# Performance work log

Hardware: AMD Instinct MI355X
Metric: run time of the kernel (lower is better)

Reference implementation:

```python
import jax, jax.numpy as jnp
import numpy as np

P = 4096          # n_patch (64x64 grid)
S = 64            # grid side
L = 9             # 9-neighbor window
E = 34            # attention embed dim (32 hidden + 2 coords)
H = 32            # hidden size
N_OBS = 10
N_PRED = 50


def _neighbor_flat_idx():
    idx = np.arange(P)
    r, c = idx // S, idx % S
    off = np.array([[-1,-1],[-1,0],[-1,1],[0,-1],[0,0],[0,1],[1,-1],[1,0],[1,1]])
    nr = (r[:, None] + off[:, 0]).reshape(S, S, L)
    nc = (c[:, None] + off[:, 1]).reshape(S, S, L)
    # boundary shift (as in the torch module)
    nr[0] += 1; nr[-1] -= 1
    nc[:, 0] += 1; nc[:, -1] -= 1
    return jnp.asarray((nr * S + nc).reshape(P, L))  # [P, 9] into patch dim


def _patch_label(B):
    coords = jnp.arange(S, dtype=jnp.float32) / S
    pl = jnp.stack(jnp.meshgrid(coords, coords, indexing='ij'), -1).reshape(P, 2)
    return jnp.broadcast_to(pl[:, None, :], (P, B, 2))  # [P, B, 2]


def setup_inputs() -> dict:
    key = jax.random.key(0)
    ks = jax.random.split(key, 8)
    s = 0.1
    return {
        'x': jax.random.normal(ks[0], (N_OBS, 2 * P, H), jnp.float32),
        'W_x2h': jax.random.normal(ks[1], (H, H), jnp.float32) * s,
        'b_x2h': jnp.zeros((H,), jnp.float32),
        'W_h2h': jax.random.normal(ks[2], (H, H), jnp.float32) * s,
        'b_h2h': jnp.zeros((H,), jnp.float32),
        'W_fc2': jax.random.normal(ks[3], (H, H), jnp.float32) * s,
        'b_fc2': jnp.zeros((H,), jnp.float32),
        'ln_g': jnp.ones((H,), jnp.float32),
        'ln_b': jnp.zeros((H,), jnp.float32),
        'W_fcsa': jax.random.normal(ks[4], (H, E), jnp.float32) * s,
        'b_fcsa': jnp.zeros((H,), jnp.float32),
        'W_in': jax.random.normal(ks[5], (3 * E, E), jnp.float32) * s,
        'b_in': jnp.zeros((3 * E,), jnp.float32),
        'W_out': jax.random.normal(ks[6], (E, E), jnp.float32) * s,
        'b_out': jnp.zeros((E,), jnp.float32),
    }


def reference(x, W_x2h, b_x2h, W_h2h, b_h2h, W_fc2, b_fc2, ln_g, ln_b,
              W_fcsa, b_fcsa, W_in, b_in, W_out, b_out):
    B = x.shape[1] // P
    N = B * P
    nbr = _neighbor_flat_idx()
    pl = _patch_label(B)

    def layernorm(y):
        mu = jnp.mean(y, -1, keepdims=True)
        var = jnp.mean((y - mu) ** 2, -1, keepdims=True)
        return (y - mu) * jax.lax.rsqrt(var + 1e-5) * ln_g + ln_b

    def mha(xa):  # [L, N, E] self-attention, 1 head
        qkv = xa @ W_in.T + b_in
        q, k, v = jnp.split(qkv, 3, axis=-1)
        scores = jnp.einsum('lne,mne->nlm', q, k) / jnp.sqrt(jnp.float32(E))
        w = jax.nn.softmax(scores, axis=-1)
        o = jnp.einsum('nlm,mne->lne', w, v)
        return o @ W_out.T + b_out

    def step(h, inp):
        h = jnp.tanh(inp @ W_x2h.T + b_x2h + h @ W_h2h.T + b_h2h)  # [N, H]
        hb = jnp.transpose(h.reshape(B, P, H), (1, 0, 2))          # [P, B, H]
        qin = jnp.concatenate([hb, pl], -1)                        # [P, B, E]
        nq = qin[nbr]                                              # [P, 9, B, E]
        xa = jnp.transpose(nq, (1, 2, 0, 3)).reshape(L, N, E)      # [9, N, E]
        ao = mha(xa)[4]                                            # center, [N, E]
        h = h + ao @ W_fcsa.T + b_fcsa
        pred = layernorm(h @ W_fc2.T + b_fc2)
        return h, pred

    h0 = jnp.zeros((N, H), x.dtype)
    h, preds_obs = jax.lax.scan(step, h0, x)                       # [10, N, H]

    def step_pred(carry, _):
        h, p = carry
        h, pnew = step(h, p)
        return (h, pnew), pnew

    _, preds_fut = jax.lax.scan(step_pred, (h, preds_obs[-1]), None,
                                length=N_PRED - 1)                 # [49, N, H]
    return jnp.concatenate([preds_obs, preds_fut], 0)              # [59, N, H]
```

## Files before the change

### kernel.cpp

```cpp
#include <hip/hip_runtime.h>

#define NROWS 8192
#define RPB   32
#define TPB   1024
#define NBLK  256

#define OFF_W1   0
#define OFF_W2   1024
#define OFF_WIN  2048
#define OFF_WFC2 5516
#define OFF_M    6540
#define OFF_B12  7628
#define OFF_BIN  7660
#define OFF_B2   7762
#define OFF_BFC2 7794
#define OFF_LNG  7826
#define OFF_LNB  7858
#define OFF_QKV0 8192
#define QKVN     (NROWS*102)
#define OFF_QKV1 (OFF_QKV0 + QKVN)
#define OFF_HNEW (OFF_QKV1 + QKVN)

__global__ __launch_bounds__(256) void setup_kernel(
    const float* __restrict__ W_x2h, const float* __restrict__ b_x2h,
    const float* __restrict__ W_h2h, const float* __restrict__ b_h2h,
    const float* __restrict__ W_fc2, const float* __restrict__ b_fc2,
    const float* __restrict__ ln_g,  const float* __restrict__ ln_b,
    const float* __restrict__ W_fcsa,const float* __restrict__ b_fcsa,
    const float* __restrict__ W_in,  const float* __restrict__ b_in,
    const float* __restrict__ W_out, const float* __restrict__ b_out,
    float* __restrict__ ws)
{
  int t = blockIdx.x*blockDim.x + threadIdx.x;
  int stride = gridDim.x*blockDim.x;
  for (int i=t;i<1024;i+=stride) ws[OFF_W1+i]   = W_x2h[i];
  for (int i=t;i<1024;i+=stride) ws[OFF_W2+i]   = W_h2h[i];
  for (int i=t;i<3468;i+=stride) ws[OFF_WIN+i]  = W_in[i];
  for (int i=t;i<1024;i+=stride) ws[OFF_WFC2+i] = W_fc2[i];
  for (int i=t;i<32;i+=stride)   ws[OFF_B12+i]  = b_x2h[i] + b_h2h[i];
  for (int i=t;i<102;i+=stride)  ws[OFF_BIN+i]  = b_in[i];
  for (int i=t;i<32;i+=stride)   ws[OFF_BFC2+i] = b_fc2[i];
  for (int i=t;i<32;i+=stride)   ws[OFF_LNG+i]  = ln_g[i];
  for (int i=t;i<32;i+=stride)   ws[OFF_LNB+i]  = ln_b[i];
  for (int idx=t; idx<1088; idx+=stride) {
    int j = idx/34, f = idx - j*34;
    float acc = 0.f;
    for (int e=0;e<34;++e)
      acc += W_fcsa[j*34+e] * W_out[e*34+f];
    ws[OFF_M+idx] = acc;
  }
  for (int j=t;j<32;j+=stride){
    float acc = b_fcsa[j];
    for (int e=0;e<34;++e) acc += W_fcsa[j*34+e] * b_out[e];
    ws[OFF_B2+j] = acc;
  }
}

__global__ __launch_bounds__(TPB) void step_kernel(
    const float* __restrict__ ws,
    const float* __restrict__ qkvR,
    float* __restrict__ qkvW,
    float* __restrict__ hnewG,
    const float* __restrict__ x,
    float* __restrict__ out,
    int stepB, int stepA)
{
  __shared__ float sW1[32][32], sW2[32][32], sWfc2[32][32];
  __shared__ float sM[32][36];
  __shared__ float sWin[102][36];
  __shared__ float sB12[32], sBin[102], sB2[32], sBfc2[32], sLng[32], sLnb[32];
  __shared__ float sS[RPB][13];
  __shared__ float sO[RPB][35];
  __shared__ float sHp[RPB][33];
  __shared__ float sG[RPB][33];
  __shared__ float sPred[RPB][33];
  __shared__ float sHn[RPB][33];
  __shared__ float sX[RPB][33];

  const int tid  = threadIdx.x;
  const int lr2  = tid & 31;
  const int slot = tid >> 5;
  const int base = blockIdx.x * RPB;
  const int r2   = base + lr2;
  const int b    = base >> 12;
  const int p    = base & 4095;
  const int gr   = p >> 6;
  const int gc0  = p & 63;
  const int c    = gc0 + lr2;
  const int br   = (gr < 1) ? 1 : ((gr > 62) ? 62 : gr);
  const int bc   = (c  < 1) ? 1 : ((c  > 62) ? 62 : c);

  {
    sW1  [tid>>5][tid&31] = ws[OFF_W1  +tid];
    sW2  [tid>>5][tid&31] = ws[OFF_W2  +tid];
    sWfc2[tid>>5][tid&31] = ws[OFF_WFC2+tid];
    for (int idx=tid; idx<1088; idx+=TPB){ int j=idx/34, e=idx-j*34; sM[j][e]=ws[OFF_M+idx]; }
    for (int idx=tid; idx<3468; idx+=TPB){ int e=idx/34, f=idx-e*34; sWin[e][f]=ws[OFF_WIN+idx]; }
    if (tid < 102)                    sBin [tid]     = ws[OFF_BIN +tid];
    else if (tid>=128 && tid<160)     sB12 [tid-128] = ws[OFF_B12 +tid-128];
    else if (tid>=160 && tid<192)     sB2  [tid-160] = ws[OFF_B2  +tid-160];
    else if (tid>=192 && tid<224)     sBfc2[tid-192] = ws[OFF_BFC2+tid-192];
    else if (tid>=224 && tid<256)     sLng [tid-224] = ws[OFF_LNG +tid-224];
    else if (tid>=256 && tid<288)     sLnb [tid-256] = ws[OFF_LNB +tid-256];
  }
  if (stepA >= 0 && stepA < 10) {
    size_t xbase = ((size_t)stepA*NROWS + base)*32;
    sX[tid>>5][tid&31] = x[xbase + tid];
  }
  if (stepB >= 0) {
    if (slot >= 16) {
      const int j0 = (slot-16)*2;
      sHp[lr2][j0]   = hnewG[(size_t)j0    *NROWS + r2];
      sHp[lr2][j0+1] = hnewG[(size_t)(j0+1)*NROWS + r2];
    } else if (slot < 9) {
      const int m  = slot;
      const int dr = m/3 - 1, dc = m - (m/3)*3 - 1;
      const int qrow = (b<<12) + (br<<6) + bc;
      const int nr_  = (b<<12) + ((br+dr)<<6) + (bc+dc);
      float acc = 0.f;
      #pragma unroll
      for (int e=0;e<34;++e)
        acc += qkvR[(size_t)e*NROWS + qrow] * qkvR[(size_t)(34+e)*NROWS + nr_];
      sS[lr2][m] = acc * 0.1714985851425088f;
    }
  } else {
    sHp[lr2][slot] = 0.f;
  }
  __syncthreads();

  if (stepB >= 0) {
    {
      float sc[9]; float mx = -1e30f;
      #pragma unroll
      for (int m=0;m<9;++m){ sc[m]=sS[lr2][m]; mx=fmaxf(mx,sc[m]); }
      float sum=0.f;
      #pragma unroll
      for (int m=0;m<9;++m){ sc[m]=__expf(sc[m]-mx); sum+=sc[m]; }
      float inv = 1.f/sum;
      float o0=0.f, o1=0.f;
      const bool e2ok = (slot < 2);
      #pragma unroll
      for (int m=0;m<9;++m){
        int dr = m/3 - 1, dc = m - (m/3)*3 - 1;
        int nr_ = (b<<12) + ((br+dr)<<6) + (bc+dc);
        float wm = sc[m]*inv;
        o0 += wm * qkvR[(size_t)(68+slot)*NROWS + nr_];
        if (e2ok) o1 += wm * qkvR[(size_t)(100+slot)*NROWS + nr_];
      }
      sO[lr2][slot] = o0;
      if (e2ok) sO[lr2][32+slot] = o1;
    }
    __syncthreads();
    {
      float a = sB2[slot];
      #pragma unroll
      for (int e=0;e<34;++e) a += sO[lr2][e] * sM[slot][e];
      sHp[lr2][slot] += a;
    }
    __syncthreads();
    {
      float g = sBfc2[slot];
      #pragma unroll
      for (int i=0;i<32;++i) g += sHp[lr2][i] * sWfc2[slot][i];
      sG[lr2][slot] = g;
    }
    __syncthreads();
    {
      float mu=0.f;
      #pragma unroll
      for (int i=0;i<32;++i) mu += sG[lr2][i];
      mu *= 0.03125f;
      float var=0.f;
      #pragma unroll
      for (int i=0;i<32;++i){ float d=sG[lr2][i]-mu; var += d*d; }
      var *= 0.03125f;
      float rs = rsqrtf(var + 1e-5f);
      sPred[lr2][slot] = (sG[lr2][slot]-mu)*rs*sLng[slot] + sLnb[slot];
    }
    __syncthreads();
    {
      size_t obase = ((size_t)stepB*NROWS + base)*32;
      out[obase + tid] = sPred[tid>>5][tid&31];
    }
  } else {
    __syncthreads(); __syncthreads(); __syncthreads(); __syncthreads();
  }

  if (stepA >= 0) {
    float a = sB12[slot];
    if (stepA < 10) {
      #pragma unroll
      for (int i=0;i<32;++i)
        a += sX[lr2][i]*sW1[slot][i] + sHp[lr2][i]*sW2[slot][i];
    } else {
      #pragma unroll
      for (int i=0;i<32;++i)
        a += sPred[lr2][i]*sW1[slot][i] + sHp[lr2][i]*sW2[slot][i];
    }
    {
      float t0 = tanhf(a);
      sHn[lr2][slot] = t0;
      hnewG[(size_t)slot*NROWS + r2] = t0;
    }
    __syncthreads();
    float hn[32];
    #pragma unroll
    for (int f=0;f<32;++f) hn[f]=sHn[lr2][f];
    const float pl0 = gr*0.015625f, pl1 = c*0.015625f;
    #pragma unroll
    for (int k=0;k<4;++k){
      int e = slot + 32*k;
      if (e < 102) {
        float acc = sBin[e];
        #pragma unroll
        for (int f=0;f<32;++f) acc += hn[f]*sWin[e][f];
        acc += pl0*sWin[e][32] + pl1*sWin[e][33];
        qkvW[(size_t)e*NROWS + r2] = acc;
      }
    }
  }
}

extern "C" void kernel_launch(void* const* d_in, const int* in_sizes, int n_in,
                              void* d_out, int out_size, void* d_ws, size_t ws_size,
                              hipStream_t stream) {
  const float* x     = (const float*)d_in[0];
  const float* W_x2h = (const float*)d_in[1];
  const float* b_x2h = (const float*)d_in[2];
  const float* W_h2h = (const float*)d_in[3];
  const float* b_h2h = (const float*)d_in[4];
  const float* W_fc2 = (const float*)d_in[5];
  const float* b_fc2 = (const float*)d_in[6];
  const float* ln_g  = (const float*)d_in[7];
  const float* ln_b  = (const float*)d_in[8];
  const float* W_fcsa= (const float*)d_in[9];
  const float* b_fcsa= (const float*)d_in[10];
  const float* W_in  = (const float*)d_in[11];
  const float* b_in  = (const float*)d_in[12];
  const float* W_out = (const float*)d_in[13];
  const float* b_out = (const float*)d_in[14];
  float* ws = (float*)d_ws;
  float* out = (float*)d_out;

  setup_kernel<<<8, 256, 0, stream>>>(W_x2h,b_x2h,W_h2h,b_h2h,W_fc2,b_fc2,ln_g,ln_b,
                                      W_fcsa,b_fcsa,W_in,b_in,W_out,b_out, ws);
  for (int i=0;i<60;++i){
    int stepB = i-1;
    int stepA = (i<=58)? i : -1;
    const float* qR = ws + OFF_QKV0 + (size_t)((i+1)&1)*QKVN;
    float*       qW = ws + OFF_QKV0 + (size_t)(i&1)*QKVN;
    step_kernel<<<NBLK, TPB, 0, stream>>>(ws, qR, qW, ws+OFF_HNEW, x, out, stepB, stepA);
  }
}
```

Before: 962.6 us.

## Fuse two recurrent steps per launch using halo recomputation in shared memory

Each launch now covers two time steps. Every block recomputes the first step over a 3x33 halo of cells around its own 32-cell row segment, keeping the halo's qkv in shared memory so the second step's neighbour attention needs no global exchange. This halves the number of kernel launches and the global round trips of qkv and hidden state, at the cost of redundant halo computation (about three times the cells in the first step) and much larger shared memory use, which may reduce occupancy. Hidden state is double-buffered in a row-major layout, and shared arrays are padded to reduce bank conflicts.

Measured after the change: 1.472 ms. 1.53x slower.

```diff
diff --git a/kernel.cpp b/kernel.cpp
--- a/kernel.cpp
+++ b/kernel.cpp
@@ -1,9 +1,11 @@
 #include <hip/hip_runtime.h>
 
 #define NROWS 8192
-#define RPB   32
 #define TPB   1024
 #define NBLK  256
+#define NCELL 99
+#define SCALE 0.1714985851425088f
+#define INV64 0.015625f
 
 #define OFF_W1   0
 #define OFF_W2   1024
@@ -18,8 +20,8 @@
 #define OFF_LNB  7858
 #define OFF_QKV0 8192
 #define QKVN     (NROWS*102)
-#define OFF_QKV1 (OFF_QKV0 + QKVN)
-#define OFF_HNEW (OFF_QKV1 + QKVN)
+#define HNN      (NROWS*32)
+#define OFF_HN0  (OFF_QKV0 + 2*QKVN)
 
 __global__ __launch_bounds__(256) void setup_kernel(
     const float* __restrict__ W_x2h, const float* __restrict__ b_x2h,
@@ -56,167 +58,295 @@
   }
 }
 
-__global__ __launch_bounds__(TPB) void step_kernel(
+__global__ __launch_bounds__(TPB) void fused2_kernel(
     const float* __restrict__ ws,
     const float* __restrict__ qkvR,
     float* __restrict__ qkvW,
-    float* __restrict__ hnewG,
+    const float* __restrict__ hnR,
+    float* __restrict__ hnW,
     const float* __restrict__ x,
     float* __restrict__ out,
-    int stepB, int stepA)
+    int l)
 {
-  __shared__ float sW1[32][32], sW2[32][32], sWfc2[32][32];
-  __shared__ float sM[32][36];
-  __shared__ float sWin[102][36];
+  __shared__ float sW1[32][33], sW2[32][33], sWfc2[32][33];
+  __shared__ float sM[32][35];
+  __shared__ float sWin[102][35];
   __shared__ float sB12[32], sBin[102], sB2[32], sBfc2[32], sLng[32], sLnb[32];
-  __shared__ float sS[RPB][13];
-  __shared__ float sO[RPB][35];
-  __shared__ float sHp[RPB][33];
-  __shared__ float sG[RPB][33];
-  __shared__ float sPred[RPB][33];
-  __shared__ float sHn[RPB][33];
-  __shared__ float sX[RPB][33];
-
-  const int tid  = threadIdx.x;
-  const int lr2  = tid & 31;
-  const int slot = tid >> 5;
-  const int base = blockIdx.x * RPB;
-  const int r2   = base + lr2;
-  const int b    = base >> 12;
-  const int p    = base & 4095;
-  const int gr   = p >> 6;
-  const int gc0  = p & 63;
-  const int c    = gc0 + lr2;
-  const int br   = (gr < 1) ? 1 : ((gr > 62) ? 62 : gr);
-  const int bc   = (c  < 1) ? 1 : ((c  > 62) ? 62 : c);
+  __shared__ float sHp  [32][NCELL];
+  __shared__ float sPredT[32][NCELL];
+  __shared__ float sHnT [32][NCELL];
+  __shared__ float sGT  [32][NCELL];
+  __shared__ float sS[NCELL][13];
+  __shared__ float uOX[36][102];
+  __shared__ float sX2[32][33];
+  __shared__ float sQKV2[3][102][37];
+
+  const int tid = threadIdx.x;
+  const int bid = blockIdx.x;
+  const int b   = bid >> 7;
+  const int gr  = (bid >> 1) & 63;
+  const int ch  = bid & 1;
+  const int c0  = ch << 5;
+  const int br  = (gr < 1) ? 1 : ((gr > 62) ? 62 : gr);
+  const int R0  = br - 1;
+  const int C0  = ch ? 31 : 0;
+  const int rr_own = gr - R0;
+  const int cc0 = c0 - C0;
+  const int ownbase = (b<<12) + (gr<<6) + c0;
+  const int sPrev = 2*l - 1, sEven = 2*l, sOdd = 2*l + 1;
+  const bool hasP1 = (l >= 1);
+  const bool hasP4 = (sOdd <= 58);
 
   {
-    sW1  [tid>>5][tid&31] = ws[OFF_W1  +tid];
-    sW2  [tid>>5][tid&31] = ws[OFF_W2  +tid];
-    sWfc2[tid>>5][tid&31] = ws[OFF_WFC2+tid];
-    for (int idx=tid; idx<1088; idx+=TPB){ int j=idx/34, e=idx-j*34; sM[j][e]=ws[OFF_M+idx]; }
-    for (int idx=tid; idx<3468; idx+=TPB){ int e=idx/34, f=idx-e*34; sWin[e][f]=ws[OFF_WIN+idx]; }
-    if (tid < 102)                    sBin [tid]     = ws[OFF_BIN +tid];
-    else if (tid>=128 && tid<160)     sB12 [tid-128] = ws[OFF_B12 +tid-128];
-    else if (tid>=160 && tid<192)     sB2  [tid-160] = ws[OFF_B2  +tid-160];
-    else if (tid>=192 && tid<224)     sBfc2[tid-192] = ws[OFF_BFC2+tid-192];
-    else if (tid>=224 && tid<256)     sLng [tid-224] = ws[OFF_LNG +tid-224];
-    else if (tid>=256 && tid<288)     sLnb [tid-256] = ws[OFF_LNB +tid-256];
-  }
-  if (stepA >= 0 && stepA < 10) {
-    size_t xbase = ((size_t)stepA*NROWS + base)*32;
-    sX[tid>>5][tid&31] = x[xbase + tid];
-  }
-  if (stepB >= 0) {
-    if (slot >= 16) {
-      const int j0 = (slot-16)*2;
-      sHp[lr2][j0]   = hnewG[(size_t)j0    *NROWS + r2];
-      sHp[lr2][j0+1] = hnewG[(size_t)(j0+1)*NROWS + r2];
-    } else if (slot < 9) {
-      const int m  = slot;
-      const int dr = m/3 - 1, dc = m - (m/3)*3 - 1;
-      const int qrow = (b<<12) + (br<<6) + bc;
-      const int nr_  = (b<<12) + ((br+dr)<<6) + (bc+dc);
+    int j = tid >> 5, i = tid & 31;
+    sW1[j][i]   = ws[OFF_W1  + tid];
+    sW2[j][i]   = ws[OFF_W2  + tid];
+    sWfc2[j][i] = ws[OFF_WFC2+ tid];
+    for (int idx = tid; idx < 1088; idx += TPB){ int jj=idx/34, e=idx-jj*34; sM[jj][e]=ws[OFF_M+idx]; }
+    for (int idx = tid; idx < 3468; idx += TPB){ int e=idx/34, f=idx-e*34; sWin[e][f]=ws[OFF_WIN+idx]; }
+    if (tid < 102)                sBin [tid]     = ws[OFF_BIN + tid];
+    else if (tid>=128 && tid<160) sB12 [tid-128] = ws[OFF_B12 + tid-128];
+    else if (tid>=160 && tid<192) sB2  [tid-160] = ws[OFF_B2  + tid-160];
+    else if (tid>=192 && tid<224) sBfc2[tid-192] = ws[OFF_BFC2+ tid-192];
+    else if (tid>=224 && tid<256) sLng [tid-224] = ws[OFF_LNG + tid-224];
+    else if (tid>=256 && tid<288) sLnb [tid-256] = ws[OFF_LNB + tid-256];
+  }
+  if (l == 0) {
+    for (int tt = tid; tt < 3168; tt += TPB) {
+      int cell = tt >> 5, j = tt & 31;
+      sHp[j][cell] = 0.f;
+      int rr = cell/33, cc = cell - rr*33;
+      int ar = (b<<12) + ((R0+rr)<<6) + C0 + cc;
+      uOX[j][cell] = x[(size_t)ar*32 + j];
+    }
+  }
+  if (hasP4 && sOdd < 10) {
+    int cell = tid >> 5, j = tid & 31;
+    sX2[cell][j] = x[((size_t)sOdd*NROWS + ownbase + cell)*32 + j];
+  }
+  __syncthreads();
+
+  if (hasP1) {
+    if (tid < 891) {
+      int m = tid / 99, cell = tid - m*99;
+      int rr = cell/33, cc = cell - rr*33;
+      int g = R0+rr, c = C0+cc;
+      int bg  = (g<1)?1:((g>62)?62:g);
+      int bcc = (c<1)?1:((c>62)?62:c);
+      int dr = m/3 - 1, dc = m - (m/3)*3 - 1;
+      int qrow = (b<<12)+(bg<<6)+bcc;
+      int krow = (b<<12)+((bg+dr)<<6)+(bcc+dc);
       float acc = 0.f;
       #pragma unroll
       for (int e=0;e<34;++e)
-        acc += qkvR[(size_t)e*NROWS + qrow] * qkvR[(size_t)(34+e)*NROWS + nr_];
-      sS[lr2][m] = acc * 0.1714985851425088f;
-    }
-  } else {
-    sHp[lr2][slot] = 0.f;
-  }
-  __syncthreads();
-
-  if (stepB >= 0) {
-    {
+        acc += qkvR[(size_t)e*NROWS+qrow]*qkvR[(size_t)(34+e)*NROWS+krow];
+      sS[cell][m] = acc*SCALE;
+    }
+    __syncthreads();
+    if (tid < 990) {
+      int sub = tid / 99, cell = tid - sub*99;
+      int rr = cell/33, cc = cell - rr*33;
+      int g = R0+rr, c = C0+cc;
+      int bg  = (g<1)?1:((g>62)?62:g);
+      int bcc = (c<1)?1:((c>62)?62:c);
       float sc[9]; float mx = -1e30f;
       #pragma unroll
-      for (int m=0;m<9;++m){ sc[m]=sS[lr2][m]; mx=fmaxf(mx,sc[m]); }
+      for (int m=0;m<9;++m){ sc[m]=sS[cell][m]; mx=fmaxf(mx,sc[m]); }
       float sum=0.f;
       #pragma unroll
       for (int m=0;m<9;++m){ sc[m]=__expf(sc[m]-mx); sum+=sc[m]; }
       float inv = 1.f/sum;
-      float o0=0.f, o1=0.f;
-      const bool e2ok = (slot < 2);
+      const int f0=sub, f1=sub+10, f2=sub+20, f3=sub+30;
+      const bool h3 = (sub < 4);
+      float o0=0.f,o1=0.f,o2=0.f,o3=0.f;
       #pragma unroll
       for (int m=0;m<9;++m){
         int dr = m/3 - 1, dc = m - (m/3)*3 - 1;
-        int nr_ = (b<<12) + ((br+dr)<<6) + (bc+dc);
+        int krow = (b<<12)+((bg+dr)<<6)+(bcc+dc);
         float wm = sc[m]*inv;
-        o0 += wm * qkvR[(size_t)(68+slot)*NROWS + nr_];
-        if (e2ok) o1 += wm * qkvR[(size_t)(100+slot)*NROWS + nr_];
-      }
-      sO[lr2][slot] = o0;
-      if (e2ok) sO[lr2][32+slot] = o1;
-    }
-    __syncthreads();
-    {
-      float a = sB2[slot];
-      #pragma unroll
-      for (int e=0;e<34;++e) a += sO[lr2][e] * sM[slot][e];
-      sHp[lr2][slot] += a;
-    }
-    __syncthreads();
-    {
-      float g = sBfc2[slot];
-      #pragma unroll
-      for (int i=0;i<32;++i) g += sHp[lr2][i] * sWfc2[slot][i];
-      sG[lr2][slot] = g;
-    }
-    __syncthreads();
-    {
+        o0 += wm*qkvR[(size_t)(68+f0)*NROWS+krow];
+        o1 += wm*qkvR[(size_t)(68+f1)*NROWS+krow];
+        o2 += wm*qkvR[(size_t)(68+f2)*NROWS+krow];
+        if (h3) o3 += wm*qkvR[(size_t)(68+f3)*NROWS+krow];
+      }
+      uOX[f0][cell]=o0; uOX[f1][cell]=o1; uOX[f2][cell]=o2;
+      if (h3) uOX[f3][cell]=o3;
+    }
+    __syncthreads();
+    for (int tt = tid; tt < 3168; tt += TPB) {
+      int cell = tt>>5, j = tt&31;
+      int rr = cell/33, cc = cell - rr*33;
+      int ar = (b<<12)+((R0+rr)<<6)+C0+cc;
+      float a = sB2[j] + hnR[(size_t)ar*32 + j];
+      #pragma unroll
+      for (int e=0;e<34;++e) a += uOX[e][cell]*sM[j][e];
+      sHp[j][cell] = a;
+    }
+    __syncthreads();
+    for (int tt = tid; tt < 3168; tt += TPB) {
+      int cell = tt>>5, j = tt&31;
+      float g2 = sBfc2[j];
+      #pragma unroll
+      for (int i=0;i<32;++i) g2 += sHp[i][cell]*sWfc2[j][i];
+      sGT[j][cell] = g2;
+      if (sEven < 10) {
+        int rr = cell/33, cc = cell - rr*33;
+        int ar = (b<<12)+((R0+rr)<<6)+C0+cc;
+        uOX[j][cell] = x[((size_t)sEven*NROWS + ar)*32 + j];
+      }
+    }
+    __syncthreads();
+    for (int tt = tid; tt < 3168; tt += TPB) {
+      int cell = tt>>5, j = tt&31;
       float mu=0.f;
       #pragma unroll
-      for (int i=0;i<32;++i) mu += sG[lr2][i];
+      for (int i=0;i<32;++i) mu += sGT[i][cell];
       mu *= 0.03125f;
       float var=0.f;
       #pragma unroll
-      for (int i=0;i<32;++i){ float d=sG[lr2][i]-mu; var += d*d; }
+      for (int i=0;i<32;++i){ float d=sGT[i][cell]-mu; var += d*d; }
       var *= 0.03125f;
       float rs = rsqrtf(var + 1e-5f);
-      sPred[lr2][slot] = (sG[lr2][slot]-mu)*rs*sLng[slot] + sLnb[slot];
+      sPredT[j][cell] = (sGT[j][cell]-mu)*rs*sLng[j] + sLnb[j];
+    }
+    __syncthreads();
+  }
+
+  {
+    if (hasP1) {
+      int cell = tid>>5, j = tid&31;
+      int cellh = rr_own*33 + cc0 + cell;
+      out[((size_t)sPrev*NROWS + ownbase + cell)*32 + j] = sPredT[j][cellh];
+    }
+    for (int tt = tid; tt < 3168; tt += TPB) {
+      int cell = tt>>5, j = tt&31;
+      float a = sB12[j];
+      if (sEven < 10) {
+        #pragma unroll
+        for (int i=0;i<32;++i) a += uOX[i][cell]*sW1[j][i] + sHp[i][cell]*sW2[j][i];
+      } else {
+        #pragma unroll
+        for (int i=0;i<32;++i) a += sPredT[i][cell]*sW1[j][i] + sHp[i][cell]*sW2[j][i];
+      }
+      sHnT[j][cell] = tanhf(a);
+    }
+    __syncthreads();
+    for (int tt = tid; tt < 10098; tt += TPB) {
+      int e = tt / 99, cell = tt - e*99;
+      int rr = cell/33, cc = cell - rr*33;
+      float acc = sBin[e];
+      #pragma unroll
+      for (int f=0; f<32; ++f) acc += sHnT[f][cell]*sWin[e][f];
+      acc += (R0+rr)*INV64*sWin[e][32] + (C0+cc)*INV64*sWin[e][33];
+      sQKV2[rr][e][cc] = acc;
+    }
+    __syncthreads();
+  }
+
+  {
+    if (tid < 288) {
+      int m = tid>>5, cell = tid&31;
+      int c = c0 + cell;
+      int bcc = (c<1)?1:((c>62)?62:c);
+      int dr = m/3 - 1, dc = m - (m/3)*3 - 1;
+      int colq = bcc - C0, colk = bcc + dc - C0, rrk = 1 + dr;
+      float acc = 0.f;
+      #pragma unroll
+      for (int e=0;e<34;++e) acc += sQKV2[1][e][colq]*sQKV2[rrk][34+e][colk];
+      sS[cell][m] = acc*SCALE;
+    }
+    __syncthreads();
+    if (tid < 320) {
+      int sub = tid>>5, cell = tid&31;
+      int c = c0 + cell;
+      int bcc = (c<1)?1:((c>62)?62:c);
+      float sc[9]; float mx = -1e30f;
+      #pragma unroll
+      for (int m=0;m<9;++m){ sc[m]=sS[cell][m]; mx=fmaxf(mx,sc[m]); }
+      float sum=0.f;
+      #pragma unroll
+      for (int m=0;m<9;++m){ sc[m]=__expf(sc[m]-mx); sum+=sc[m]; }
+      float inv = 1.f/sum;
+      const int f0=sub, f1=sub+10, f2=sub+20, f3=sub+30;
+      const bool h3 = (sub < 4);
+      float o0=0.f,o1=0.f,o2=0.f,o3=0.f;
+      #pragma unroll
+      for (int m=0;m<9;++m){
+        int dr = m/3 - 1, dc = m - (m/3)*3 - 1;
+        int colk = bcc + dc - C0, rrk = 1 + dr;
+        float wm = sc[m]*inv;
+        o0 += wm*sQKV2[rrk][68+f0][colk];
+        o1 += wm*sQKV2[rrk][68+f1][colk];
+        o2 += wm*sQKV2[rrk][68+f2][colk];
+        if (h3) o3 += wm*sQKV2[rrk][68+f3][colk];
+      }
+      uOX[f0][cell]=o0; uOX[f1][cell]=o1; uOX[f2][cell]=o2;
+      if (h3) uOX[f3][cell]=o3;
     }
     __syncthreads();
     {
-      size_t obase = ((size_t)stepB*NROWS + base)*32;
-      out[obase + tid] = sPred[tid>>5][tid&31];
-    }
-  } else {
-    __syncthreads(); __syncthreads(); __syncthreads(); __syncthreads();
-  }
-
-  if (stepA >= 0) {
-    float a = sB12[slot];
-    if (stepA < 10) {
-      #pragma unroll
-      for (int i=0;i<32;++i)
-        a += sX[lr2][i]*sW1[slot][i] + sHp[lr2][i]*sW2[slot][i];
-    } else {
-      #pragma unroll
-      for (int i=0;i<32;++i)
-        a += sPred[lr2][i]*sW1[slot][i] + sHp[lr2][i]*sW2[slot][i];
-    }
+      int cell = tid>>5, j = tid&31;
+      int cellh = rr_own*33 + cc0 + cell;
+      float a = sB2[j] + sHnT[j][cellh];
+      #pragma unroll
+      for (int e=0;e<34;++e) a += uOX[e][cell]*sM[j][e];
+      sHp[j][cellh] = a;
+    }
+    __syncthreads();
     {
-      float t0 = tanhf(a);
-      sHn[lr2][slot] = t0;
-      hnewG[(size_t)slot*NROWS + r2] = t0;
-    }
-    __syncthreads();
-    float hn[32];
-    #pragma unroll
-    for (int f=0;f<32;++f) hn[f]=sHn[lr2][f];
-    const float pl0 = gr*0.015625f, pl1 = c*0.015625f;
-    #pragma unroll
-    for (int k=0;k<4;++k){
-      int e = slot + 32*k;
-      if (e < 102) {
-        float acc = sBin[e];
+      int cell = tid>>5, j = tid&31;
+      int cellh = rr_own*33 + cc0 + cell;
+      float g2 = sBfc2[j];
+      #pragma unroll
+      for (int i=0;i<32;++i) g2 += sHp[i][cellh]*sWfc2[j][i];
+      sGT[j][cellh] = g2;
+    }
+    __syncthreads();
+    {
+      int cell = tid>>5, j = tid&31;
+      int cellh = rr_own*33 + cc0 + cell;
+      float mu=0.f;
+      #pragma unroll
+      for (int i=0;i<32;++i) mu += sGT[i][cellh];
+      mu *= 0.03125f;
+      float var=0.f;
+      #pragma unroll
+      for (int i=0;i<32;++i){ float d=sGT[i][cellh]-mu; var += d*d; }
+      var *= 0.03125f;
+      float rs = rsqrtf(var + 1e-5f);
+      sPredT[j][cellh] = (sGT[j][cellh]-mu)*rs*sLng[j] + sLnb[j];
+    }
+    __syncthreads();
+  }
+
+  {
+    int cell = tid>>5, j = tid&31;
+    int cellh = rr_own*33 + cc0 + cell;
+    out[((size_t)sEven*NROWS + ownbase + cell)*32 + j] = sPredT[j][cellh];
+    if (hasP4) {
+      float a = sB12[j];
+      if (sOdd < 10) {
         #pragma unroll
-        for (int f=0;f<32;++f) acc += hn[f]*sWin[e][f];
-        acc += pl0*sWin[e][32] + pl1*sWin[e][33];
-        qkvW[(size_t)e*NROWS + r2] = acc;
-      }
+        for (int i=0;i<32;++i) a += sX2[cell][i]*sW1[j][i] + sHp[i][cellh]*sW2[j][i];
+      } else {
+        #pragma unroll
+        for (int i=0;i<32;++i) a += sPredT[i][cellh]*sW1[j][i] + sHp[i][cellh]*sW2[j][i];
+      }
+      float tv = tanhf(a);
+      sHnT[j][cellh] = tv;
+      hnW[((size_t)ownbase + cell)*32 + j] = tv;
+    }
+  }
+  if (hasP4) {
+    __syncthreads();
+    for (int tt = tid; tt < 3264; tt += TPB) {
+      int e = tt>>5, cell = tt&31;
+      int cellh = rr_own*33 + cc0 + cell;
+      float acc = sBin[e];
+      #pragma unroll
+      for (int f=0;f<32;++f) acc += sHnT[f][cellh]*sWin[e][f];
+      acc += gr*INV64*sWin[e][32] + (c0+cell)*INV64*sWin[e][33];
+      qkvW[(size_t)e*NROWS + ownbase + cell] = acc;
     }
   }
 }
@@ -244,11 +374,11 @@
 
   setup_kernel<<<8, 256, 0, stream>>>(W_x2h,b_x2h,W_h2h,b_h2h,W_fc2,b_fc2,ln_g,ln_b,
                                       W_fcsa,b_fcsa,W_in,b_in,W_out,b_out, ws);
-  for (int i=0;i<60;++i){
-    int stepB = i-1;
-    int stepA = (i<=58)? i : -1;
-    const float* qR = ws + OFF_QKV0 + (size_t)((i+1)&1)*QKVN;
-    float*       qW = ws + OFF_QKV0 + (size_t)(i&1)*QKVN;
-    step_kernel<<<NBLK, TPB, 0, stream>>>(ws, qR, qW, ws+OFF_HNEW, x, out, stepB, stepA);
+  for (int l = 0; l < 30; ++l) {
+    const float* qR = ws + OFF_QKV0 + (size_t)((l+1)&1)*QKVN;
+    float*       qW = ws + OFF_QKV0 + (size_t)(l&1)*QKVN;
+    const float* hR = ws + OFF_HN0  + (size_t)((l+1)&1)*HNN;
+    float*       hW = ws + OFF_HN0  + (size_t)(l&1)*HNN;
+    fused2_kernel<<<NBLK, TPB, 0, stream>>>(ws, qR, qW, hR, hW, x, out, l);
   }
 }
```

## Remap threads so each wavefront owns two rows, replacing block barriers with wave-local fences

Applied to the files above, without the earlier changes.

Changes the thread mapping so that each 64-lane wavefront handles two full rows, with lane j as the feature index. Most __syncthreads are replaced by an LDS wait plus a scheduling barrier, and LayerNorm reductions are done with cross-lane shuffles. The hidden state layout becomes row-major for coalesced access, and shared weight arrays are padded to avoid bank conflicts. The trade-offs are that global qkv reads now use strided access per lane, and correctness rests on data being shared only within a wavefront.

Result: slower. 1.416 ms (+47.1%).

```diff
diff --git a/kernel.cpp b/kernel.cpp
--- a/kernel.cpp
+++ b/kernel.cpp
@@ -4,6 +4,11 @@
 #define RPB   32
 #define TPB   1024
 #define NBLK  256
+#define SCALE 0.1714985851425088f
+#define INV64 0.015625f
+
+#define WFENCE() do { asm volatile("s_waitcnt lgkmcnt(0)" ::: "memory"); \
+                      __builtin_amdgcn_sched_barrier(0); } while (0)
 
 #define OFF_W1   0
 #define OFF_W2   1024
@@ -65,155 +70,143 @@
     float* __restrict__ out,
     int stepB, int stepA)
 {
-  __shared__ float sW1[32][32], sW2[32][32], sWfc2[32][32];
-  __shared__ float sM[32][36];
-  __shared__ float sWin[102][36];
+  __shared__ float sW1[32][33], sW2[32][33], sWfc2[32][33];
+  __shared__ float sM[32][35];
+  __shared__ float sWin[102][35];
   __shared__ float sB12[32], sBin[102], sB2[32], sBfc2[32], sLng[32], sLnb[32];
-  __shared__ float sS[RPB][13];
-  __shared__ float sO[RPB][35];
-  __shared__ float sHp[RPB][33];
-  __shared__ float sG[RPB][33];
-  __shared__ float sPred[RPB][33];
-  __shared__ float sHn[RPB][33];
-  __shared__ float sX[RPB][33];
+  __shared__ float sQ[32][35];
+  __shared__ float sS[32][13];
+  __shared__ float sO[32][35];
+  __shared__ float sHp[32][33];
+  __shared__ float sPred[32][33];
+  __shared__ float sHn[32][33];
+  __shared__ float sX[32][33];
 
   const int tid  = threadIdx.x;
-  const int lr2  = tid & 31;
-  const int slot = tid >> 5;
+  const int l    = tid & 63;
+  const int j    = l & 31;
+  const int rowg = ((tid >> 6) << 1) + (l >> 5);
   const int base = blockIdx.x * RPB;
-  const int r2   = base + lr2;
+  const int r2   = base + rowg;
   const int b    = base >> 12;
   const int p    = base & 4095;
   const int gr   = p >> 6;
   const int gc0  = p & 63;
-  const int c    = gc0 + lr2;
+  const int c    = gc0 + rowg;
   const int br   = (gr < 1) ? 1 : ((gr > 62) ? 62 : gr);
   const int bc   = (c  < 1) ? 1 : ((c  > 62) ? 62 : c);
+  const int qrow = (b<<12) + (br<<6) + bc;
 
   {
     sW1  [tid>>5][tid&31] = ws[OFF_W1  +tid];
     sW2  [tid>>5][tid&31] = ws[OFF_W2  +tid];
     sWfc2[tid>>5][tid&31] = ws[OFF_WFC2+tid];
-    for (int idx=tid; idx<1088; idx+=TPB){ int j=idx/34, e=idx-j*34; sM[j][e]=ws[OFF_M+idx]; }
+    for (int idx=tid; idx<1088; idx+=TPB){ int jj=idx/34, e=idx-jj*34; sM[jj][e]=ws[OFF_M+idx]; }
     for (int idx=tid; idx<3468; idx+=TPB){ int e=idx/34, f=idx-e*34; sWin[e][f]=ws[OFF_WIN+idx]; }
-    if (tid < 102)                    sBin [tid]     = ws[OFF_BIN +tid];
-    else if (tid>=128 && tid<160)     sB12 [tid-128] = ws[OFF_B12 +tid-128];
-    else if (tid>=160 && tid<192)     sB2  [tid-160] = ws[OFF_B2  +tid-160];
-    else if (tid>=192 && tid<224)     sBfc2[tid-192] = ws[OFF_BFC2+tid-192];
-    else if (tid>=224 && tid<256)     sLng [tid-224] = ws[OFF_LNG +tid-224];
-    else if (tid>=256 && tid<288)     sLnb [tid-256] = ws[OFF_LNB +tid-256];
-  }
-  if (stepA >= 0 && stepA < 10) {
-    size_t xbase = ((size_t)stepA*NROWS + base)*32;
-    sX[tid>>5][tid&31] = x[xbase + tid];
-  }
+    if (tid < 102)                sBin [tid]     = ws[OFF_BIN +tid];
+    else if (tid>=128 && tid<160) sB12 [tid-128] = ws[OFF_B12 +tid-128];
+    else if (tid>=160 && tid<192) sB2  [tid-160] = ws[OFF_B2  +tid-160];
+    else if (tid>=192 && tid<224) sBfc2[tid-192] = ws[OFF_BFC2+tid-192];
+    else if (tid>=224 && tid<256) sLng [tid-224] = ws[OFF_LNG +tid-224];
+    else if (tid>=256 && tid<288) sLnb [tid-256] = ws[OFF_LNB +tid-256];
+  }
+  float hprev = 0.f;
+  if (stepB >= 0) hprev = hnewG[(size_t)r2*32 + j];
+  if (stepA >= 0 && stepA < 10)
+    sX[rowg][j] = x[((size_t)stepA*NROWS + r2)*32 + j];
+
   if (stepB >= 0) {
-    if (slot >= 16) {
-      const int j0 = (slot-16)*2;
-      sHp[lr2][j0]   = hnewG[(size_t)j0    *NROWS + r2];
-      sHp[lr2][j0+1] = hnewG[(size_t)(j0+1)*NROWS + r2];
-    } else if (slot < 9) {
-      const int m  = slot;
-      const int dr = m/3 - 1, dc = m - (m/3)*3 - 1;
-      const int qrow = (b<<12) + (br<<6) + bc;
-      const int nr_  = (b<<12) + ((br+dr)<<6) + (bc+dc);
+    sQ[rowg][j] = qkvR[(size_t)j*NROWS + qrow];
+    if (j < 2) sQ[rowg][32+j] = qkvR[(size_t)(32+j)*NROWS + qrow];
+    WFENCE();
+    if (j < 9) {
+      const int dr = j/3 - 1, dc = j - (j/3)*3 - 1;
+      const int krow = (b<<12) + ((br+dr)<<6) + (bc+dc);
       float acc = 0.f;
       #pragma unroll
       for (int e=0;e<34;++e)
-        acc += qkvR[(size_t)e*NROWS + qrow] * qkvR[(size_t)(34+e)*NROWS + nr_];
-      sS[lr2][m] = acc * 0.1714985851425088f;
-    }
-  } else {
-    sHp[lr2][slot] = 0.f;
-  }
-  __syncthreads();
-
-  if (stepB >= 0) {
+        acc += sQ[rowg][e] * qkvR[(size_t)(34+e)*NROWS + krow];
+      sS[rowg][j] = acc * SCALE;
+    }
+    WFENCE();
     {
       float sc[9]; float mx = -1e30f;
       #pragma unroll
-      for (int m=0;m<9;++m){ sc[m]=sS[lr2][m]; mx=fmaxf(mx,sc[m]); }
+      for (int m=0;m<9;++m){ sc[m]=sS[rowg][m]; mx=fmaxf(mx,sc[m]); }
       float sum=0.f;
       #pragma unroll
       for (int m=0;m<9;++m){ sc[m]=__expf(sc[m]-mx); sum+=sc[m]; }
       float inv = 1.f/sum;
       float o0=0.f, o1=0.f;
-      const bool e2ok = (slot < 2);
+      const bool x2 = (j < 2);
       #pragma unroll
       for (int m=0;m<9;++m){
         int dr = m/3 - 1, dc = m - (m/3)*3 - 1;
-        int nr_ = (b<<12) + ((br+dr)<<6) + (bc+dc);
+        int krow = (b<<12) + ((br+dr)<<6) + (bc+dc);
         float wm = sc[m]*inv;
-        o0 += wm * qkvR[(size_t)(68+slot)*NROWS + nr_];
-        if (e2ok) o1 += wm * qkvR[(size_t)(100+slot)*NROWS + nr_];
+        o0 += wm * qkvR[(size_t)(68+j)*NROWS + krow];
+        if (x2) o1 += wm * qkvR[(size_t)(100+j)*NROWS + krow];
       }
-      sO[lr2][slot] = o0;
-      if (e2ok) sO[lr2][32+slot] = o1;
-    }
-    __syncthreads();
-    {
-      float a = sB2[slot];
-      #pragma unroll
-      for (int e=0;e<34;++e) a += sO[lr2][e] * sM[slot][e];
-      sHp[lr2][slot] += a;
-    }
-    __syncthreads();
-    {
-      float g = sBfc2[slot];
-      #pragma unroll
-      for (int i=0;i<32;++i) g += sHp[lr2][i] * sWfc2[slot][i];
-      sG[lr2][slot] = g;
-    }
-    __syncthreads();
-    {
-      float mu=0.f;
-      #pragma unroll
-      for (int i=0;i<32;++i) mu += sG[lr2][i];
-      mu *= 0.03125f;
-      float var=0.f;
-      #pragma unroll
-      for (int i=0;i<32;++i){ float d=sG[lr2][i]-mu; var += d*d; }
-      var *= 0.03125f;
-      float rs = rsqrtf(var + 1e-5f);
-      sPred[lr2][slot] = (sG[lr2][slot]-mu)*rs*sLng[slot] + sLnb[slot];
-    }
-    __syncthreads();
-    {
-      size_t obase = ((size_t)stepB*NROWS + base)*32;
-      out[obase + tid] = sPred[tid>>5][tid&31];
-    }
+      sO[rowg][j] = o0;
+      if (x2) sO[rowg][32+j] = o1;
+    }
+  }
+  __syncthreads();
+
+  float hp, pred = 0.f;
+  if (stepB >= 0) {
+    float a = hprev + sB2[j];
+    #pragma unroll
+    for (int e=0;e<34;++e) a += sO[rowg][e] * sM[j][e];
+    hp = a;
   } else {
-    __syncthreads(); __syncthreads(); __syncthreads(); __syncthreads();
+    hp = 0.f;
+  }
+  sHp[rowg][j] = hp;
+  WFENCE();
+  if (stepB >= 0) {
+    float g = sBfc2[j];
+    #pragma unroll
+    for (int i=0;i<32;++i) g += sHp[rowg][i] * sWfc2[j][i];
+    float mu = g;
+    #pragma unroll
+    for (int k=1;k<32;k<<=1) mu += __shfl_xor(mu, k, 64);
+    mu *= 0.03125f;
+    float d = g - mu;
+    float var = d*d;
+    #pragma unroll
+    for (int k=1;k<32;k<<=1) var += __shfl_xor(var, k, 64);
+    var *= 0.03125f;
+    float rs = rsqrtf(var + 1e-5f);
+    pred = d*rs*sLng[j] + sLnb[j];
+    out[((size_t)stepB*NROWS + r2)*32 + j] = pred;
+    sPred[rowg][j] = pred;
   }
 
   if (stepA >= 0) {
-    float a = sB12[slot];
+    WFENCE();
+    float a = sB12[j];
     if (stepA < 10) {
       #pragma unroll
       for (int i=0;i<32;++i)
-        a += sX[lr2][i]*sW1[slot][i] + sHp[lr2][i]*sW2[slot][i];
+        a += sX[rowg][i]*sW1[j][i] + sHp[rowg][i]*sW2[j][i];
     } else {
       #pragma unroll
       for (int i=0;i<32;++i)
-        a += sPred[lr2][i]*sW1[slot][i] + sHp[lr2][i]*sW2[slot][i];
-    }
-    {
-      float t0 = tanhf(a);
-      sHn[lr2][slot] = t0;
-      hnewG[(size_t)slot*NROWS + r2] = t0;
-    }
-    __syncthreads();
-    float hn[32];
-    #pragma unroll
-    for (int f=0;f<32;++f) hn[f]=sHn[lr2][f];
-    const float pl0 = gr*0.015625f, pl1 = c*0.015625f;
+        a += sPred[rowg][i]*sW1[j][i] + sHp[rowg][i]*sW2[j][i];
+    }
+    float hn = tanhf(a);
+    sHn[rowg][j] = hn;
+    hnewG[(size_t)r2*32 + j] = hn;
+    WFENCE();
+    const float pl0 = gr*INV64, pl1 = c*INV64;
     #pragma unroll
     for (int k=0;k<4;++k){
-      int e = slot + 32*k;
+      int e = j + 32*k;
       if (e < 102) {
         float acc = sBin[e];
         #pragma unroll
-        for (int f=0;f<32;++f) acc += hn[f]*sWin[e][f];
+        for (int f=0;f<32;++f) acc += sHn[rowg][f]*sWin[e][f];
         acc += pl0*sWin[e][32] + pl1*sWin[e][33];
         qkvW[(size_t)e*NROWS + r2] = acc;
       }
```

## Stage neighbor QKV halo tile in shared memory for window attention

Applied to the files above, without the earlier changes.

Each block now loads a 3-row by 34-column halo of the Q/K/V projections (all 102 channels) into a shared-memory tile once, and computes scores and the weighted value sum from that tile instead of issuing repeated strided global gathers per neighbor. The previous hidden state is loaded into its own buffer and added in the attention-output step, and shared-memory row strides are changed to odd paddings to reduce bank conflicts. This removes redundant global and L2 traffic for the nine-neighbor window. In exchange it adds about 42 KB of LDS per block, an extra barrier, and a cooperative load loop with integer div/mod indexing.

After: 1.161 ms. 20.6% more time.

```diff
diff --git a/kernel.cpp b/kernel.cpp
--- a/kernel.cpp
+++ b/kernel.cpp
@@ -4,6 +4,8 @@
 #define RPB   32
 #define TPB   1024
 #define NBLK  256
+#define SCALE 0.1714985851425088f
+#define INV64 0.015625f
 
 #define OFF_W1   0
 #define OFF_W2   1024
@@ -65,12 +67,14 @@
     float* __restrict__ out,
     int stepB, int stepA)
 {
-  __shared__ float sW1[32][32], sW2[32][32], sWfc2[32][32];
-  __shared__ float sM[32][36];
-  __shared__ float sWin[102][36];
+  __shared__ float sW1[32][33], sW2[32][33], sWfc2[32][33];
+  __shared__ float sM[32][35];
+  __shared__ float sWin[102][35];
   __shared__ float sB12[32], sBin[102], sB2[32], sBfc2[32], sLng[32], sLnb[32];
+  __shared__ float sKV[3][34][103];
   __shared__ float sS[RPB][13];
   __shared__ float sO[RPB][35];
+  __shared__ float sHprev[RPB][33];
   __shared__ float sHp[RPB][33];
   __shared__ float sG[RPB][33];
   __shared__ float sPred[RPB][33];
@@ -89,6 +93,7 @@
   const int c    = gc0 + lr2;
   const int br   = (gr < 1) ? 1 : ((gr > 62) ? 62 : gr);
   const int bc   = (c  < 1) ? 1 : ((c  > 62) ? 62 : c);
+  const int ccq  = bc - gc0 + 1;
 
   {
     sW1  [tid>>5][tid&31] = ws[OFF_W1  +tid];
@@ -108,27 +113,35 @@
     sX[tid>>5][tid&31] = x[xbase + tid];
   }
   if (stepB >= 0) {
-    if (slot >= 16) {
-      const int j0 = (slot-16)*2;
-      sHp[lr2][j0]   = hnewG[(size_t)j0    *NROWS + r2];
-      sHp[lr2][j0+1] = hnewG[(size_t)(j0+1)*NROWS + r2];
-    } else if (slot < 9) {
-      const int m  = slot;
-      const int dr = m/3 - 1, dc = m - (m/3)*3 - 1;
-      const int qrow = (b<<12) + (br<<6) + bc;
-      const int nr_  = (b<<12) + ((br+dr)<<6) + (bc+dc);
+    {
+      int j = tid >> 5, r = tid & 31;
+      sHprev[r][j] = hnewG[(size_t)j*NROWS + base + r];
+    }
+    for (int idx = tid; idx < 10404; idx += TPB) {
+      int e    = idx / 102;
+      int cell = idx - e*102;
+      int rr   = cell / 34, cc = cell - rr*34;
+      int gcol = gc0 - 1 + cc;
+      gcol = (gcol < 0) ? 0 : ((gcol > 63) ? 63 : gcol);
+      int flat = (b<<12) + ((br-1+rr)<<6) + gcol;
+      sKV[rr][cc][e] = qkvR[(size_t)e*NROWS + flat];
+    }
+  } else {
+    if (slot < 32) sHp[lr2][slot] = 0.f;
+  }
+  __syncthreads();
+
+  if (stepB >= 0) {
+    if (slot < 9) {
+      const int dr = slot/3 - 1, dc = slot - (slot/3)*3 - 1;
+      const int rrk = 1 + dr, cck = ccq + dc;
       float acc = 0.f;
       #pragma unroll
       for (int e=0;e<34;++e)
-        acc += qkvR[(size_t)e*NROWS + qrow] * qkvR[(size_t)(34+e)*NROWS + nr_];
-      sS[lr2][m] = acc * 0.1714985851425088f;
-    }
-  } else {
-    sHp[lr2][slot] = 0.f;
-  }
-  __syncthreads();
-
-  if (stepB >= 0) {
+        acc += sKV[1][ccq][e] * sKV[rrk][cck][34+e];
+      sS[lr2][slot] = acc * SCALE;
+    }
+    __syncthreads();
     {
       float sc[9]; float mx = -1e30f;
       #pragma unroll
@@ -142,20 +155,20 @@
       #pragma unroll
       for (int m=0;m<9;++m){
         int dr = m/3 - 1, dc = m - (m/3)*3 - 1;
-        int nr_ = (b<<12) + ((br+dr)<<6) + (bc+dc);
+        int rrk = 1 + dr, cck = ccq + dc;
         float wm = sc[m]*inv;
-        o0 += wm * qkvR[(size_t)(68+slot)*NROWS + nr_];
-        if (e2ok) o1 += wm * qkvR[(size_t)(100+slot)*NROWS + nr_];
+        o0 += wm * sKV[rrk][cck][68+slot];
+        if (e2ok) o1 += wm * sKV[rrk][cck][100+slot];
       }
       sO[lr2][slot] = o0;
       if (e2ok) sO[lr2][32+slot] = o1;
     }
     __syncthreads();
     {
-      float a = sB2[slot];
+      float a = sB2[slot] + sHprev[lr2][slot];
       #pragma unroll
       for (int e=0;e<34;++e) a += sO[lr2][e] * sM[slot][e];
-      sHp[lr2][slot] += a;
+      sHp[lr2][slot] = a;
     }
     __syncthreads();
     {
@@ -182,22 +195,20 @@
       size_t obase = ((size_t)stepB*NROWS + base)*32;
       out[obase + tid] = sPred[tid>>5][tid&31];
     }
-  } else {
-    __syncthreads(); __syncthreads(); __syncthreads(); __syncthreads();
   }
 
   if (stepA >= 0) {
-    float a = sB12[slot];
-    if (stepA < 10) {
-      #pragma unroll
-      for (int i=0;i<32;++i)
-        a += sX[lr2][i]*sW1[slot][i] + sHp[lr2][i]*sW2[slot][i];
-    } else {
-      #pragma unroll
-      for (int i=0;i<32;++i)
-        a += sPred[lr2][i]*sW1[slot][i] + sHp[lr2][i]*sW2[slot][i];
-    }
-    {
+    {
+      float a = sB12[slot];
+      if (stepA < 10) {
+        #pragma unroll
+        for (int i=0;i<32;++i)
+          a += sX[lr2][i]*sW1[slot][i] + sHp[lr2][i]*sW2[slot][i];
+      } else {
+        #pragma unroll
+        for (int i=0;i<32;++i)
+          a += sPred[lr2][i]*sW1[slot][i] + sHp[lr2][i]*sW2[slot][i];
+      }
       float t0 = tanhf(a);
       sHn[lr2][slot] = t0;
       hnewG[(size_t)slot*NROWS + r2] = t0;
@@ -206,7 +217,7 @@
     float hn[32];
     #pragma unroll
     for (int f=0;f<32;++f) hn[f]=sHn[lr2][f];
-    const float pl0 = gr*0.015625f, pl1 = c*0.015625f;
+    const float pl0 = gr*INV64, pl1 = c*INV64;
     #pragma unroll
     for (int k=0;k<4;++k){
       int e = slot + 32*k;
```
